# Kernel optimization log

Measured on AMD Instinct MI355X. Metric: run time of the kernel, lower is better.

Reference implementation:

```python
import jax, jax.numpy as jnp
import numpy as np

IDIM = 128   # idim == odim (fc1 input dim must match shift-slice width idim_q)
HDIM = 1024
CDIM = 256
IGNORE_OUT = 10000.0


def setup_inputs() -> dict:
    key = jax.random.key(0)
    ks = jax.random.split(key, 4)
    B, T = 4, 512
    x = jax.random.normal(ks[0], (B, T, IDIM), dtype=jnp.float32)
    y = jax.random.normal(ks[1], (B, T, IDIM), dtype=jnp.float32)
    # xavier-ish init for the two linears (bias zeroed, as in initialize())
    w1 = jax.random.normal(ks[2], (HDIM, IDIM), dtype=jnp.float32) / np.sqrt(IDIM).astype(np.float32)
    b1 = jnp.zeros((HDIM,), jnp.float32)
    w2 = jax.random.normal(ks[3], (IDIM, HDIM), dtype=jnp.float32) / np.sqrt(HDIM).astype(np.float32)
    b2 = jnpts = jnp.zeros((IDIM,), jnp.float32)
    return {"x": x, "y": y, "w1": w1, "b1": b1, "w2": w2, "b2": b2}


def _shift_stack(key_seq, idim):
    """Vectorized _pad_for_shift: (B,T,idim) -> (B,T,2*idim-1,idim) shifted slices."""
    pad = idim - 1
    kp = jnp.pad(key_seq, ((0, 0), (0, 0), (pad, pad)))  # (B,T,3*idim-2)
    idx = jnp.arange(2 * idim - 1)[:, None] + jnp.arange(idim)[None, :]  # (S, idim)
    return kp[..., idx]  # (B,T,S,idim)


def _forward(x, y, w1, b1, w2, b2):
    idim = IDIM
    n_iter = HDIM // CDIM
    seq_mask = (y == IGNORE_OUT)                      # (B,T,odim)
    denom = jnp.sum(~seq_mask).astype(x.dtype)
    y_res, x_res = y, x
    losses = []
    for i in range(n_iter):
        # --- argaug (scale=False): sliding cosine cross-correlation + argmax ---
        kpt = _shift_stack(x_res, idim)               # (B,T,S,idim), S=2*idim-1
        num = jnp.einsum('btd,btsd->bts', y_res, kpt)
        den = jnp.linalg.norm(y_res, axis=-1)[..., None] * jnp.linalg.norm(kpt, axis=-1)
        sim = jnp.where(den == 0, 0.0, num / jnp.where(den == 0, 1.0, den))  # NaN(0/0) -> 0
        idx = jnp.argmax(sim, axis=-1)                # (B,T), first max like torch.max
        x_aug = jnp.take_along_axis(kpt, idx[..., None, None], axis=2)[..., 0, :]  # (B,T,idim)
        # --- attention (detached) ---
        attn = jax.lax.stop_gradient(jax.nn.softmax(x_aug * y_res, axis=-1))
        x_attn = x_aug * attn
        # --- _reverse_pad_for_shift: un-shift x_attn by 2*idim-2 - idx ---
        pad = idim - 1
        xap = jnp.pad(x_attn, ((0, 0), (0, 0), (pad, pad)))
        ridx = (2 * idim - 2 - idx)[..., None] + jnp.arange(idim)  # (B,T,idim)
        x_ele = jnp.take_along_axis(xap, ridx, axis=-1)
        # --- channel-masked two-layer MLP ---
        h = x_attn @ w1.T + b1                        # (B,T,hdim)
        m = jnp.zeros((HDIM,), x.dtype).at[i * CDIM:(i + 1) * CDIM].set(1.0)
        y_ele = (h * m) @ w2.T + b2                   # (B,T,odim)
        # --- masked MSE (sum of masked squared errors / #unmasked) ---
        sq = jnp.where(seq_mask, 0.0, (y_ele - y_res) ** 2)
        losses.append(jnp.sum(sq) / denom)
        y_res = y_res - y_ele
        x_res = x_res - x_ele
    return jnp.mean(jnp.stack(losses))


def reference(x, y, w1, b1, w2, b2):
    return _forward(x, y, w1, b1, w2, b2)
```

## Files before the change

kernel.cpp:

```cpp
#include <hip/hip_runtime.h>
#include <math.h>

#define NROWS 2048
#define NBLK  2048
#define NITER 4
#define IGNORE_OUT 10000.0f

__device__ __forceinline__ float readlanef(float v, int lane){
  return __int_as_float(__builtin_amdgcn_readlane(__float_as_int(v), lane));
}
__device__ __forceinline__ float rotup1(float v){
  int i = __float_as_int(v);
  return __int_as_float(__builtin_amdgcn_update_dpp(i, i, 0x13C, 0xF, 0xF, false));
}
__device__ __forceinline__ float gather128(float v0, float v1, int idx){
  float g0 = __shfl(v0, idx & 63, 64);
  float g1 = __shfl(v1, idx & 63, 64);
  float r  = (idx & 64) ? g1 : g0;
  return ((unsigned)idx < 128u) ? r : 0.f;
}
__device__ __forceinline__ float bflySum(float v){
  #pragma unroll
  for (int o = 32; o; o >>= 1) v += __shfl_xor(v, o, 64);
  return v;
}
__device__ __forceinline__ float bflyMax(float v){
  #pragma unroll
  for (int o = 32; o; o >>= 1) v = fmaxf(v, __shfl_xor(v, o, 64));
  return v;
}

__global__ __launch_bounds__(128)
void prepK(const float* __restrict__ w1, const float* __restrict__ b1,
           const float* __restrict__ w2, const float* __restrict__ b2,
           float* __restrict__ M4, float* __restrict__ biasT, int* __restrict__ ticket){
  const int blk = blockIdx.x;
  const int u = threadIdx.x;
  if (blk < 512){
    int i = blk >> 7, o = blk & 127;
    const float* w1p = w1 + (i * 256) * 128 + u;
    const float* w2p = w2 + o * 1024 + i * 256;
    float a = 0.f;
    #pragma unroll 16
    for (int c = 0; c < 256; ++c) a = fmaf(w1p[c * 128], w2p[c], a);
    M4[i * 16384 + (u >> 2) * 512 + o * 4 + (u & 3)] = a;
  } else if (blk < 516){
    int i = blk - 512;
    const float* w2p = w2 + u * 1024 + i * 256;
    const float* b1p = b1 + i * 256;
    float a = b2[u];
    #pragma unroll 8
    for (int c = 0; c < 256; ++c) a = fmaf(b1p[c], w2p[c], a);
    biasT[i * 128 + u] = a;
  } else {
    if (u == 0) *ticket = 0;
  }
}

__global__ __launch_bounds__(128, 4)
void mainK(const float* __restrict__ x, const float* __restrict__ y,
           const float* __restrict__ M4, const float* __restrict__ biasT,
           unsigned long long* __restrict__ partials, int* __restrict__ ticket,
           float* __restrict__ out){
  __shared__ float sVal[2];
  __shared__ int   sIdx[2];
  __shared__ float yel[128];
  __shared__ float sL[2], sC[2];
  __shared__ int   sOld;

  const int u = threadIdx.x;
  const int l = u & 63;
  const int w = u >> 6;
  const bool isl0 = (l == 0);
  const long base = (long)blockIdx.x * 128;

  float xlo = x[base + l],      xhi = x[base + 64 + l];
  float ylo = y[base + l],      yhi = y[base + 64 + l];
  const bool mlo = (ylo == IGNORE_OUT), mhi = (yhi == IGNORE_OUT);
  const bool ownM = w ? mhi : mlo;
  float cnt = ownM ? 0.f : 1.f;
  float lossAcc = 0.f;

  for (int i = 0; i < NITER; ++i){
    float sq_lo = xlo * xlo, sq_hi = xhi * xhi;
    float v = w ? sq_hi : sq_lo;
    #pragma unroll
    for (int o2 = 1; o2 < 64; o2 <<= 1){
      float tv = __shfl_up(v, o2, 64);
      if (l >= o2) v += tv;
    }
    float osum  = bflySum(w ? sq_lo : sq_hi);
    float total = readlanef(v, 63) + osum;
    float pref_t = w ? (v + osum) : v;

    float nY = sqrtf(bflySum(ylo * ylo + yhi * yhi));

    float nt = 0.f, n1 = 0.f;
    {
      float src0 = w ? ylo : yhi;
      float win = __shfl(src0, 63 - l, 64);
      if (w == 0){
        #pragma unroll 8
        for (int j = 0; j < 64; ++j){
          float sx = readlanef(xlo, j);
          nt = fmaf(win, sx, nt);
          n1 = (j == l) ? nt : n1;
          float inc = readlanef(ylo, j);
          float r = rotup1(win);
          win = isl0 ? inc : r;
        }
        #pragma unroll 8
        for (int j = 0; j < 64; ++j){
          float sx = readlanef(xhi, j);
          nt = fmaf(win, sx, nt);
          float inc = readlanef(yhi, j);
          float r = rotup1(win);
          win = isl0 ? inc : r;
        }
      } else {
        #pragma unroll 8
        for (int j = 0; j < 64; ++j){
          float sx = readlanef(xlo, j);
          nt = fmaf(win, sx, nt);
          float inc = readlanef(yhi, j);
          float r = rotup1(win);
          win = isl0 ? inc : r;
        }
        #pragma unroll 8
        for (int j = 0; j < 64; ++j){
          float sx = readlanef(xhi, j);
          nt = fmaf(win, sx, nt);
          n1 = (j == l) ? nt : n1;
          float inc = readlanef(ylo, j);
          float r = rotup1(win);
          win = isl0 ? inc : r;
        }
      }
    }

    {
      float num1 = n1, num2 = nt - n1;
      float d1 = nY * sqrtf(pref_t);
      float d2 = nY * sqrtf(fmaxf(total - pref_t, 0.f));
      float s1 = (d1 == 0.f) ? 0.f : num1 / d1;
      float s2 = (d2 == 0.f) ? 0.f : num2 / d2;
      int tsh = (w << 6) | l;
      if (tsh == 127) s2 = -INFINITY;
      float bv = s1; int bi = tsh;
      if (s2 > bv){ bv = s2; bi = tsh + 128; }
      #pragma unroll
      for (int o2 = 1; o2 < 64; o2 <<= 1){
        float ov = __shfl_xor(bv, o2, 64);
        int   oi = __shfl_xor(bi, o2, 64);
        if (ov > bv || (ov == bv && oi < bi)){ bv = ov; bi = oi; }
      }
      if (l == 0){ sVal[w] = bv; sIdx[w] = bi; }
    }
    __syncthreads();
    int sstar;
    {
      float v0 = sVal[0], v1 = sVal[1];
      int   i0 = sIdx[0], i1 = sIdx[1];
      sstar = (v1 > v0 || (v1 == v0 && i1 < i0)) ? i1 : i0;
    }

    int j0 = sstar + l - 127;
    float xa = gather128(xlo, xhi, j0);
    float xb = gather128(xlo, xhi, j0 + 64);
    float za = xa * ylo, zb = xb * yhi;
    float mz = bflyMax(fmaxf(za, zb));
    float ea = expf(za - mz), eb = expf(zb - mz);
    float se = bflySum(ea + eb);
    float wlo = xa * (ea / se), whi = xb * (eb / se);

    int k0 = l + 127 - sstar;
    xlo -= gather128(wlo, whi, k0);
    xhi -= gather128(wlo, whi, k0 + 64);

    float ye;
    {
      const float4* Mp = (const float4*)(M4 + (size_t)i * 16384);
      float av = 0.f;
      #pragma unroll
      for (int dd = 0; dd < 16; ++dd){
        float4 m = Mp[dd * 128 + u];
        av = fmaf(m.x, readlanef(wlo, 4 * dd + 0), av);
        av = fmaf(m.y, readlanef(wlo, 4 * dd + 1), av);
        av = fmaf(m.z, readlanef(wlo, 4 * dd + 2), av);
        av = fmaf(m.w, readlanef(wlo, 4 * dd + 3), av);
      }
      #pragma unroll
      for (int dd = 16; dd < 32; ++dd){
        float4 m = Mp[dd * 128 + u];
        int b = 4 * dd - 64;
        av = fmaf(m.x, readlanef(whi, b + 0), av);
        av = fmaf(m.y, readlanef(whi, b + 1), av);
        av = fmaf(m.z, readlanef(whi, b + 2), av);
        av = fmaf(m.w, readlanef(whi, b + 3), av);
      }
      ye = av + biasT[i * 128 + u];
    }
    {
      float yown = w ? yhi : ylo;
      float dOwn = ye - yown;
      if (!ownM) lossAcc = fmaf(dOwn, dOwn, lossAcc);
    }
    yel[u] = ye;
    __syncthreads();
    {
      float dlo = yel[l] - ylo, dhi = yel[64 + l] - yhi;
      ylo = -dlo; yhi = -dhi;
    }
  }

  lossAcc = bflySum(lossAcc);
  cnt     = bflySum(cnt);
  if (l == 0){ sL[w] = lossAcc; sC[w] = cnt; }
  __syncthreads();
  if (u == 0){
    union { float2 f; unsigned long long v; } pk;
    pk.f.x = sL[0] + sL[1]; pk.f.y = sC[0] + sC[1];
    __hip_atomic_store(&partials[blockIdx.x], pk.v, __ATOMIC_RELEASE, __HIP_MEMORY_SCOPE_AGENT);
    sOld = __hip_atomic_fetch_add(ticket, 1, __ATOMIC_ACQ_REL, __HIP_MEMORY_SCOPE_AGENT);
  }
  __syncthreads();
  if (sOld == NBLK - 1){
    float ls = 0.f, cs = 0.f;
    for (int g = u; g < NBLK; g += 128){
      union { float2 f; unsigned long long v; } pk;
      pk.v = __hip_atomic_load(&partials[g], __ATOMIC_ACQUIRE, __HIP_MEMORY_SCOPE_AGENT);
      ls += pk.f.x; cs += pk.f.y;
    }
    ls = bflySum(ls); cs = bflySum(cs);
    if (l == 0){ sL[w] = ls; sC[w] = cs; }
    __syncthreads();
    if (u == 0) out[0] = (sL[0] + sL[1]) / ((float)NITER * (sC[0] + sC[1]));
  }
}

extern "C" void kernel_launch(void* const* d_in, const int* in_sizes, int n_in,
                              void* d_out, int out_size, void* d_ws, size_t ws_size,
                              hipStream_t stream){
  const float* x  = (const float*)d_in[0];
  const float* y  = (const float*)d_in[1];
  const float* w1 = (const float*)d_in[2];
  const float* b1 = (const float*)d_in[3];
  const float* w2 = (const float*)d_in[4];
  const float* b2 = (const float*)d_in[5];
  float* out = (float*)d_out;

  int*   ticket = (int*)d_ws;
  float* M4     = (float*)((char*)d_ws + 256);
  float* biasT  = (float*)((char*)d_ws + 256 + 4 * 128 * 128 * sizeof(float));
  unsigned long long* partials =
      (unsigned long long*)((char*)d_ws + 256 + 4 * 128 * 128 * sizeof(float) + 4 * 128 * sizeof(float));

  prepK<<<517, 128, 0, stream>>>(w1, b1, w2, b2, M4, biasT, ticket);
  mainK<<<NBLK, 128, 0, stream>>>(x, y, M4, biasT, partials, ticket, out);
}
```

Measured before the change: 166.1 us.

## Split per-row correlation and matvec across four waves, drop softmax max shift

Doubles the block to 256 threads so each row's sliding cross-correlation and the 128x128 matvec are split in half across extra waves, with partial sums combined through shared memory. This shortens the serial per-wave readlane/FMA chain and raises parallelism per row. The price is extra barriers and idle lanes in the norm and argmax stages. It also removes the max subtraction from the softmax, which saves a reduction but risks overflow for large products.

```diff
diff --git a/kernel.cpp b/kernel.cpp
--- a/kernel.cpp
+++ b/kernel.cpp
@@ -22,11 +22,6 @@
 __device__ __forceinline__ float bflySum(float v){
   #pragma unroll
   for (int o = 32; o; o >>= 1) v += __shfl_xor(v, o, 64);
-  return v;
-}
-__device__ __forceinline__ float bflyMax(float v){
-  #pragma unroll
-  for (int o = 32; o; o >>= 1) v = fmaxf(v, __shfl_xor(v, o, 64));
   return v;
 }
 
@@ -57,15 +52,17 @@
   }
 }
 
-__global__ __launch_bounds__(128, 4)
+__global__ __launch_bounds__(256, 8)
 void mainK(const float* __restrict__ x, const float* __restrict__ y,
            const float* __restrict__ M4, const float* __restrict__ biasT,
            unsigned long long* __restrict__ partials, int* __restrict__ ticket,
            float* __restrict__ out){
+  __shared__ float pNT[256];
+  __shared__ float pN1[256];
+  __shared__ float yel[128];
   __shared__ float sVal[2];
   __shared__ int   sIdx[2];
-  __shared__ float yel[128];
-  __shared__ float sL[2], sC[2];
+  __shared__ float sL[4], sC[4];
   __shared__ int   sOld;
 
   const int u = threadIdx.x;
@@ -74,80 +71,73 @@
   const bool isl0 = (l == 0);
   const long base = (long)blockIdx.x * 128;
 
-  float xlo = x[base + l],      xhi = x[base + 64 + l];
-  float ylo = y[base + l],      yhi = y[base + 64 + l];
+  float xlo = x[base + l], xhi = x[base + 64 + l];
+  float ylo = y[base + l], yhi = y[base + 64 + l];
   const bool mlo = (ylo == IGNORE_OUT), mhi = (yhi == IGNORE_OUT);
-  const bool ownM = w ? mhi : mlo;
-  float cnt = ownM ? 0.f : 1.f;
+  const bool mOwn = (w == 0) ? mlo : mhi;
+  float cnt = (u < 128 && !mOwn) ? 1.f : 0.f;
   float lossAcc = 0.f;
 
   for (int i = 0; i < NITER; ++i){
-    float sq_lo = xlo * xlo, sq_hi = xhi * xhi;
-    float v = w ? sq_hi : sq_lo;
-    #pragma unroll
-    for (int o2 = 1; o2 < 64; o2 <<= 1){
-      float tv = __shfl_up(v, o2, 64);
-      if (l >= o2) v += tv;
-    }
-    float osum  = bflySum(w ? sq_lo : sq_hi);
-    float total = readlanef(v, 63) + osum;
-    float pref_t = w ? (v + osum) : v;
-
-    float nY = sqrtf(bflySum(ylo * ylo + yhi * yhi));
-
-    float nt = 0.f, n1 = 0.f;
+    float pref_t = 0.f, total = 0.f, nY = 0.f;
+    if (w < 2){
+      float own2 = (w == 0) ? xlo * xlo : xhi * xhi;
+      float oth2 = (w == 0) ? xhi * xhi : xlo * xlo;
+      float v = own2;
+      #pragma unroll
+      for (int o2 = 1; o2 < 64; o2 <<= 1){
+        float tv = __shfl_up(v, o2, 64);
+        if (l >= o2) v += tv;
+      }
+      float osum = bflySum(oth2);
+      pref_t = (w == 0) ? v : (v + osum);
+      total  = readlanef(v, 63) + osum;
+      nY = sqrtf(bflySum(ylo * ylo + yhi * yhi));
+    }
+
     {
-      float src0 = w ? ylo : yhi;
-      float win = __shfl(src0, 63 - l, 64);
-      if (w == 0){
+      const bool a03 = (w == 0) || (w == 3);
+      float winsrc = a03 ? yhi : ylo;
+      float incSrc = a03 ? ylo : yhi;
+      float sxSrc  = (w < 2) ? xlo : xhi;
+      float win = __shfl(winsrc, 63 - l, 64);
+      float nt = 0.f, n1 = 0.f;
+      if (a03){
         #pragma unroll 8
         for (int j = 0; j < 64; ++j){
-          float sx = readlanef(xlo, j);
+          float sx = readlanef(sxSrc, j);
           nt = fmaf(win, sx, nt);
           n1 = (j == l) ? nt : n1;
-          float inc = readlanef(ylo, j);
-          float r = rotup1(win);
-          win = isl0 ? inc : r;
-        }
-        #pragma unroll 8
-        for (int j = 0; j < 64; ++j){
-          float sx = readlanef(xhi, j);
-          nt = fmaf(win, sx, nt);
-          float inc = readlanef(yhi, j);
+          float inc = readlanef(incSrc, j);
           float r = rotup1(win);
           win = isl0 ? inc : r;
         }
       } else {
         #pragma unroll 8
         for (int j = 0; j < 64; ++j){
-          float sx = readlanef(xlo, j);
+          float sx = readlanef(sxSrc, j);
           nt = fmaf(win, sx, nt);
-          float inc = readlanef(yhi, j);
+          float inc = readlanef(incSrc, j);
           float r = rotup1(win);
           win = isl0 ? inc : r;
         }
-        #pragma unroll 8
-        for (int j = 0; j < 64; ++j){
-          float sx = readlanef(xhi, j);
-          nt = fmaf(win, sx, nt);
-          n1 = (j == l) ? nt : n1;
-          float inc = readlanef(ylo, j);
-          float r = rotup1(win);
-          win = isl0 ? inc : r;
-        }
-      }
-    }
-
-    {
-      float num1 = n1, num2 = nt - n1;
+        if (w == 1) n1 = nt;
+      }
+      pNT[u] = nt; pN1[u] = n1;
+    }
+    __syncthreads();
+
+    if (w < 2){
+      float numt = pNT[u] + pNT[u + 128];
+      float num1 = pN1[u] + pN1[u + 128];
+      float num2 = numt - num1;
       float d1 = nY * sqrtf(pref_t);
       float d2 = nY * sqrtf(fmaxf(total - pref_t, 0.f));
       float s1 = (d1 == 0.f) ? 0.f : num1 / d1;
       float s2 = (d2 == 0.f) ? 0.f : num2 / d2;
-      int tsh = (w << 6) | l;
-      if (tsh == 127) s2 = -INFINITY;
-      float bv = s1; int bi = tsh;
-      if (s2 > bv){ bv = s2; bi = tsh + 128; }
+      if (u == 127) s2 = -INFINITY;
+      float bv = s1; int bi = u;
+      if (s2 > bv){ bv = s2; bi = u + 128; }
       #pragma unroll
       for (int o2 = 1; o2 < 64; o2 <<= 1){
         float ov = __shfl_xor(bv, o2, 64);
@@ -167,9 +157,7 @@
     int j0 = sstar + l - 127;
     float xa = gather128(xlo, xhi, j0);
     float xb = gather128(xlo, xhi, j0 + 64);
-    float za = xa * ylo, zb = xb * yhi;
-    float mz = bflyMax(fmaxf(za, zb));
-    float ea = expf(za - mz), eb = expf(zb - mz);
+    float ea = expf(xa * ylo), eb = expf(xb * yhi);
     float se = bflySum(ea + eb);
     float wlo = xa * (ea / se), whi = xb * (eb / se);
 
@@ -177,40 +165,33 @@
     xlo -= gather128(wlo, whi, k0);
     xhi -= gather128(wlo, whi, k0 + 64);
 
-    float ye;
     {
       const float4* Mp = (const float4*)(M4 + (size_t)i * 16384);
+      float src = (u < 128) ? wlo : whi;
+      int o = u & 127;
+      int qb = (u >> 7) * 16;
       float av = 0.f;
       #pragma unroll
-      for (int dd = 0; dd < 16; ++dd){
-        float4 m = Mp[dd * 128 + u];
-        av = fmaf(m.x, readlanef(wlo, 4 * dd + 0), av);
-        av = fmaf(m.y, readlanef(wlo, 4 * dd + 1), av);
-        av = fmaf(m.z, readlanef(wlo, 4 * dd + 2), av);
-        av = fmaf(m.w, readlanef(wlo, 4 * dd + 3), av);
-      }
-      #pragma unroll
-      for (int dd = 16; dd < 32; ++dd){
-        float4 m = Mp[dd * 128 + u];
-        int b = 4 * dd - 64;
-        av = fmaf(m.x, readlanef(whi, b + 0), av);
-        av = fmaf(m.y, readlanef(whi, b + 1), av);
-        av = fmaf(m.z, readlanef(whi, b + 2), av);
-        av = fmaf(m.w, readlanef(whi, b + 3), av);
-      }
-      ye = av + biasT[i * 128 + u];
-    }
-    {
-      float yown = w ? yhi : ylo;
-      float dOwn = ye - yown;
-      if (!ownM) lossAcc = fmaf(dOwn, dOwn, lossAcc);
-    }
-    yel[u] = ye;
-    __syncthreads();
-    {
-      float dlo = yel[l] - ylo, dhi = yel[64 + l] - yhi;
-      ylo = -dlo; yhi = -dhi;
-    }
+      for (int q = 0; q < 16; ++q){
+        float4 m = Mp[(qb + q) * 128 + o];
+        av = fmaf(m.x, readlanef(src, 4 * q + 0), av);
+        av = fmaf(m.y, readlanef(src, 4 * q + 1), av);
+        av = fmaf(m.z, readlanef(src, 4 * q + 2), av);
+        av = fmaf(m.w, readlanef(src, 4 * q + 3), av);
+      }
+      pNT[u] = av;
+    }
+    __syncthreads();
+    if (u < 128){
+      float ye = pNT[u] + pNT[u + 128] + biasT[i * 128 + u];
+      float yo = (w == 0) ? ylo : yhi;
+      float df = ye - yo;
+      if (!mOwn) lossAcc = fmaf(df, df, lossAcc);
+      yel[u] = ye;
+    }
+    __syncthreads();
+    ylo = -(yel[l] - ylo);
+    yhi = -(yel[64 + l] - yhi);
   }
 
   lossAcc = bflySum(lossAcc);
@@ -219,14 +200,15 @@
   __syncthreads();
   if (u == 0){
     union { float2 f; unsigned long long v; } pk;
-    pk.f.x = sL[0] + sL[1]; pk.f.y = sC[0] + sC[1];
+    pk.f.x = sL[0] + sL[1] + sL[2] + sL[3];
+    pk.f.y = sC[0] + sC[1] + sC[2] + sC[3];
     __hip_atomic_store(&partials[blockIdx.x], pk.v, __ATOMIC_RELEASE, __HIP_MEMORY_SCOPE_AGENT);
     sOld = __hip_atomic_fetch_add(ticket, 1, __ATOMIC_ACQ_REL, __HIP_MEMORY_SCOPE_AGENT);
   }
   __syncthreads();
   if (sOld == NBLK - 1){
     float ls = 0.f, cs = 0.f;
-    for (int g = u; g < NBLK; g += 128){
+    for (int g = u; g < NBLK; g += 256){
       union { float2 f; unsigned long long v; } pk;
       pk.v = __hip_atomic_load(&partials[g], __ATOMIC_ACQUIRE, __HIP_MEMORY_SCOPE_AGENT);
       ls += pk.f.x; cs += pk.f.y;
@@ -234,7 +216,9 @@
     ls = bflySum(ls); cs = bflySum(cs);
     if (l == 0){ sL[w] = ls; sC[w] = cs; }
     __syncthreads();
-    if (u == 0) out[0] = (sL[0] + sL[1]) / ((float)NITER * (sC[0] + sC[1]));
+    if (u == 0)
+      out[0] = (sL[0] + sL[1] + sL[2] + sL[3]) /
+               ((float)NITER * (sC[0] + sC[1] + sC[2] + sC[3]));
   }
 }
 
@@ -256,5 +240,5 @@
       (unsigned long long*)((char*)d_ws + 256 + 4 * 128 * 128 * sizeof(float) + 4 * 128 * sizeof(float));
 
   prepK<<<517, 128, 0, stream>>>(w1, b1, w2, b2, M4, biasT, ticket);
-  mainK<<<NBLK, 128, 0, stream>>>(x, y, M4, biasT, partials, ticket, out);
-}
+  mainK<<<NBLK, 256, 0, stream>>>(x, y, M4, biasT, partials, ticket, out);
+}
```

Result: no change. 168.4 us (+1.4%).
